# Kernel tuning notes

Hardware: AMD Instinct MI355X
Metric: run time of the kernel (lower is better)

## Reference

```python
import jax, jax.numpy as jnp
import numpy as np
from jax import lax

B, UNITS, IN_DIM = 1024, 4096, 256
CHI = 4  # forced: scatter writes 16 = chi*chi values per pair


def setup_inputs() -> dict:
    key = jax.random.key(0)
    k1, k2, k3 = jax.random.split(key, 3)
    inputs = jax.random.normal(k1, (B, IN_DIM), dtype=jnp.float32)
    W = jax.random.normal(k2, (UNITS, IN_DIM), dtype=jnp.float32) * 0.5  # sigma=0.5
    b = 2.0 * jnp.pi * jax.random.uniform(k3, (UNITS,), dtype=jnp.float32)
    return {"inputs": inputs, "W": W, "b": b}


def reference(inputs, W, b):
    # theta: [B, U]
    theta = inputs @ W.T + b
    half = theta * 0.5
    c = jnp.cos(half) ** 2          # R00 (real)
    s = jnp.sin(half) ** 2          # R11 (real)
    o = jnp.sin(theta) * 0.5        # imag part of R01
    z = jnp.zeros_like(c)
    R00 = lax.complex(c, z)
    R01 = lax.complex(z, o)
    R10 = lax.complex(z, -o)
    R11 = lax.complex(s, z)
    # R: [B, U, 2, 2] single-qubit rotation matrix per unit
    R = jnp.stack([jnp.stack([R00, R01], -1), jnp.stack([R10, R11], -1)], -2)
    A = R[:, 0::2]   # [B, K, 2, 2], K = U/2
    Bm = R[:, 1::2]  # [B, K, 2, 2]
    # kron(A, Bm)[2a+c, 2b+d] = A[a,b] * Bm[c,d] -> axes (a,c,b,d) then reshape
    kron = (A[:, :, :, None, :, None] * Bm[:, :, None, :, None, :]).reshape(
        A.shape[0], A.shape[1], CHI, CHI)
    # original returns (batch, chi, chi, units/2)
    return jnp.transpose(kron, (0, 2, 3, 1))
```

## Files before the change

### kernel.cpp

```cpp
#include <hip/hip_runtime.h>

#define IND   256
#define KC    32
#define WGRP  12
#define WROW  (16 * WGRP)

__global__ __launch_bounds__(256, 2)
void FeatureEncodingLayer_30374008718005_kernel(
        const float* __restrict__ X,
        const float* __restrict__ W,
        const float* __restrict__ bias,
        float* __restrict__ outf)
{
    __shared__ float Xs[KC][64];
    __shared__ float Ws[KC][WROW];

    const int tid = threadIdx.x;
    const int tx  = tid & 15;
    const int ty  = tid >> 4;

    const int kq  = tid & 7;
    const int rr  = tid >> 3;
    const int vsw = kq << 2;

    const int pt = blockIdx.x & 31;
    const int bt = blockIdx.x >> 5;

    const int b0 = bt * 64;
    const int p0 = pt * 64;
    const int u0 = p0 * 2;

    float acc[4][8];
#pragma unroll
    for (int i = 0; i < 4; ++i)
#pragma unroll
        for (int j = 0; j < 8; ++j) acc[i][j] = 0.f;

    for (int c = 0; c < IND / KC; ++c) {
        if (c) __syncthreads();
#pragma unroll
        for (int j = 0; j < 2; ++j) {
            const int r = rr + 32 * j;
            const float4 v = *reinterpret_cast<const float4*>(
                X + (size_t)(b0 + r) * IND + c * KC + kq * 4);
            const int col = r ^ vsw;
            Xs[kq * 4 + 0][col] = v.x;
            Xs[kq * 4 + 1][col] = v.y;
            Xs[kq * 4 + 2][col] = v.z;
            Xs[kq * 4 + 3][col] = v.w;
        }
#pragma unroll
        for (int j = 0; j < 4; ++j) {
            const int u = rr + 32 * j;
            const float4 v = *reinterpret_cast<const float4*>(
                W + (size_t)(u0 + u) * IND + c * KC + kq * 4);
            const int col = ((u >> 3) * WGRP + (u & 7)) ^ vsw;
            Ws[kq * 4 + 0][col] = v.x;
            Ws[kq * 4 + 1][col] = v.y;
            Ws[kq * 4 + 2][col] = v.z;
            Ws[kq * 4 + 3][col] = v.w;
        }
        __syncthreads();
#pragma unroll 8
        for (int k = 0; k < KC; ++k) {
            const int vr = ((k >> 2) & 7) << 2;
            const float4 xv = *reinterpret_cast<const float4*>(&Xs[k][(ty * 4) ^ vr]);
            const float4 wa = *reinterpret_cast<const float4*>(&Ws[k][(tx * WGRP) ^ vr]);
            const float4 wb = *reinterpret_cast<const float4*>(&Ws[k][(tx * WGRP + 4) ^ vr]);
            const float xr[4] = {xv.x, xv.y, xv.z, xv.w};
            const float wv[8] = {wa.x, wa.y, wa.z, wa.w, wb.x, wb.y, wb.z, wb.w};
#pragma unroll
            for (int rb = 0; rb < 4; ++rb)
#pragma unroll
                for (int i = 0; i < 8; ++i)
                    acc[rb][i] = fmaf(xr[rb], wv[i], acc[rb][i]);
        }
    }

    const float4 bva = *reinterpret_cast<const float4*>(bias + u0 + tx * 8);
    const float4 bvb = *reinterpret_cast<const float4*>(bias + u0 + tx * 8 + 4);
    const float bv[8] = {bva.x, bva.y, bva.z, bva.w, bvb.x, bvb.y, bvb.z, bvb.w};

#pragma unroll
    for (int rb = 0; rb < 4; ++rb) {
        const int b = b0 + ty * 4 + rb;
        float ca[4], sa[4], cb[4], sb[4], oo[4];
#pragma unroll
        for (int rp = 0; rp < 4; ++rp) {
            const float tA = acc[rb][2 * rp]     + bv[2 * rp];
            const float tB = acc[rb][2 * rp + 1] + bv[2 * rp + 1];
            float sA, cA, sB, cB;
            sincosf(tA, &sA, &cA);
            sincosf(tB, &sB, &cB);
            ca[rp] = 0.5f * (1.f + cA);
            sa[rp] = 0.5f * (1.f - cA);
            cb[rp] = 0.5f * (1.f + cB);
            sb[rp] = 0.5f * (1.f - cB);
            oo[rp] = 0.25f * sA * sB;
        }
        float* bp = outf + (size_t)b * 32768 + p0 + tx * 4;

#define STORE4(rc, EXPR) do {                                   \
        float4 v_;                                              \
        { const int rp = 0; v_.x = (EXPR); }                    \
        { const int rp = 1; v_.y = (EXPR); }                    \
        { const int rp = 2; v_.z = (EXPR); }                    \
        { const int rp = 3; v_.w = (EXPR); }                    \
        *reinterpret_cast<float4*>(bp + (rc) * 2048) = v_;      \
    } while (0)

        STORE4(0,  ca[rp] * cb[rp]);
        STORE4(1,  0.f);
        STORE4(2,  0.f);
        STORE4(3,  -oo[rp]);
        STORE4(4,  0.f);
        STORE4(5,  ca[rp] * sb[rp]);
        STORE4(6,  oo[rp]);
        STORE4(7,  0.f);
        STORE4(8,  0.f);
        STORE4(9,  oo[rp]);
        STORE4(10, sa[rp] * cb[rp]);
        STORE4(11, 0.f);
        STORE4(12, -oo[rp]);
        STORE4(13, 0.f);
        STORE4(14, 0.f);
        STORE4(15, sa[rp] * sb[rp]);
#undef STORE4
    }
}

extern "C" void kernel_launch(void* const* d_in, const int* in_sizes, int n_in,
                              void* d_out, int out_size, void* d_ws, size_t ws_size,
                              hipStream_t stream) {
    const float* X  = (const float*)d_in[0];
    const float* W  = (const float*)d_in[1];
    const float* bv = (const float*)d_in[2];

    FeatureEncodingLayer_30374008718005_kernel<<<dim3(512), dim3(256), 0, stream>>>(
        X, W, bv, (float*)d_out);
}
```

Measured before the change: 50.26 us.

## Shrink blocks to 64 threads with 8x8 register tiles and fast sincos

Changes the GEMM tiling from 256-thread blocks that compute 64x128 tiles with 4x8 per-thread outputs to 64-thread blocks that compute 64x64 tiles with 8x8 per-thread outputs, over 1024 blocks. Global loads are batched into registers before the shared-memory stores, and the swizzle is changed to match. sincosf is replaced by the fast __sincosf intrinsic. The larger register tile raises register pressure and leaves fewer waves per CU, which can hide latency less well. The fast intrinsic also loses accuracy for large arguments.

```diff
diff --git a/kernel.cpp b/kernel.cpp
--- a/kernel.cpp
+++ b/kernel.cpp
@@ -1,11 +1,9 @@
 #include <hip/hip_runtime.h>
 
-#define IND   256
-#define KC    32
-#define WGRP  12
-#define WROW  (16 * WGRP)
+#define IND 256
+#define KC  32
 
-__global__ __launch_bounds__(256, 2)
+__global__ __launch_bounds__(64, 2)
 void FeatureEncodingLayer_30374008718005_kernel(
         const float* __restrict__ X,
         const float* __restrict__ W,
@@ -13,67 +11,79 @@
         float* __restrict__ outf)
 {
     __shared__ float Xs[KC][64];
-    __shared__ float Ws[KC][WROW];
+    __shared__ float Ws[KC][64];
 
     const int tid = threadIdx.x;
-    const int tx  = tid & 15;
-    const int ty  = tid >> 4;
+    const int tx  = tid & 7;
+    const int ty  = tid >> 3;
 
     const int kq  = tid & 7;
     const int rr  = tid >> 3;
-    const int vsw = kq << 2;
+    const int sw  = kq << 3;
 
-    const int pt = blockIdx.x & 31;
-    const int bt = blockIdx.x >> 5;
-
+    const int pt = blockIdx.x & 63;
+    const int bt = blockIdx.x >> 6;
     const int b0 = bt * 64;
-    const int p0 = pt * 64;
+    const int p0 = pt * 32;
     const int u0 = p0 * 2;
 
-    float acc[4][8];
+    float acc[8][8];
 #pragma unroll
-    for (int i = 0; i < 4; ++i)
+    for (int i = 0; i < 8; ++i)
 #pragma unroll
         for (int j = 0; j < 8; ++j) acc[i][j] = 0.f;
 
     for (int c = 0; c < IND / KC; ++c) {
         if (c) __syncthreads();
+
+        float4 vx[8];
 #pragma unroll
-        for (int j = 0; j < 2; ++j) {
-            const int r = rr + 32 * j;
-            const float4 v = *reinterpret_cast<const float4*>(
+        for (int j = 0; j < 8; ++j) {
+            const int r = rr + 8 * j;
+            vx[j] = *reinterpret_cast<const float4*>(
                 X + (size_t)(b0 + r) * IND + c * KC + kq * 4);
-            const int col = r ^ vsw;
-            Xs[kq * 4 + 0][col] = v.x;
-            Xs[kq * 4 + 1][col] = v.y;
-            Xs[kq * 4 + 2][col] = v.z;
-            Xs[kq * 4 + 3][col] = v.w;
         }
 #pragma unroll
-        for (int j = 0; j < 4; ++j) {
-            const int u = rr + 32 * j;
-            const float4 v = *reinterpret_cast<const float4*>(
+        for (int j = 0; j < 8; ++j) {
+            const int col = (rr + 8 * j) ^ sw;
+            Xs[kq * 4 + 0][col] = vx[j].x;
+            Xs[kq * 4 + 1][col] = vx[j].y;
+            Xs[kq * 4 + 2][col] = vx[j].z;
+            Xs[kq * 4 + 3][col] = vx[j].w;
+        }
+        float4 vw[8];
+#pragma unroll
+        for (int j = 0; j < 8; ++j) {
+            const int u = rr + 8 * j;
+            vw[j] = *reinterpret_cast<const float4*>(
                 W + (size_t)(u0 + u) * IND + c * KC + kq * 4);
-            const int col = ((u >> 3) * WGRP + (u & 7)) ^ vsw;
-            Ws[kq * 4 + 0][col] = v.x;
-            Ws[kq * 4 + 1][col] = v.y;
-            Ws[kq * 4 + 2][col] = v.z;
-            Ws[kq * 4 + 3][col] = v.w;
+        }
+#pragma unroll
+        for (int j = 0; j < 8; ++j) {
+            const int col = (rr + 8 * j) ^ sw;
+            Ws[kq * 4 + 0][col] = vw[j].x;
+            Ws[kq * 4 + 1][col] = vw[j].y;
+            Ws[kq * 4 + 2][col] = vw[j].z;
+            Ws[kq * 4 + 3][col] = vw[j].w;
         }
         __syncthreads();
-#pragma unroll 8
+
+#pragma unroll 4
         for (int k = 0; k < KC; ++k) {
-            const int vr = ((k >> 2) & 7) << 2;
-            const float4 xv = *reinterpret_cast<const float4*>(&Xs[k][(ty * 4) ^ vr]);
-            const float4 wa = *reinterpret_cast<const float4*>(&Ws[k][(tx * WGRP) ^ vr]);
-            const float4 wb = *reinterpret_cast<const float4*>(&Ws[k][(tx * WGRP + 4) ^ vr]);
-            const float xr[4] = {xv.x, xv.y, xv.z, xv.w};
-            const float wv[8] = {wa.x, wa.y, wa.z, wa.w, wb.x, wb.y, wb.z, wb.w};
+            const int g  = (k >> 2) << 3;
+            const int xc = (ty * 8) ^ g;
+            const int wc = (tx * 8) ^ g;
+            const float4 x0 = *reinterpret_cast<const float4*>(&Xs[k][xc]);
+            const float4 x1 = *reinterpret_cast<const float4*>(&Xs[k][xc + 4]);
+            const float4 w0 = *reinterpret_cast<const float4*>(&Ws[k][wc]);
+            const float4 w1 = *reinterpret_cast<const float4*>(&Ws[k][wc + 4]);
+            const float xr[8] = {x0.x, x0.y, x0.z, x0.w, x1.x, x1.y, x1.z, x1.w};
+            const float wv[8] = {w0.x, w0.y, w0.z, w0.w, w1.x, w1.y, w1.z, w1.w};
 #pragma unroll
-            for (int rb = 0; rb < 4; ++rb)
+            for (int i = 0; i < 8; ++i)
 #pragma unroll
-                for (int i = 0; i < 8; ++i)
-                    acc[rb][i] = fmaf(xr[rb], wv[i], acc[rb][i]);
+                for (int j = 0; j < 8; ++j)
+                    acc[i][j] = fmaf(xr[i], wv[j], acc[i][j]);
         }
     }
 
@@ -82,16 +92,16 @@
     const float bv[8] = {bva.x, bva.y, bva.z, bva.w, bvb.x, bvb.y, bvb.z, bvb.w};
 
 #pragma unroll
-    for (int rb = 0; rb < 4; ++rb) {
-        const int b = b0 + ty * 4 + rb;
+    for (int rb = 0; rb < 8; ++rb) {
+        const int b = b0 + ty * 8 + rb;
         float ca[4], sa[4], cb[4], sb[4], oo[4];
 #pragma unroll
         for (int rp = 0; rp < 4; ++rp) {
             const float tA = acc[rb][2 * rp]     + bv[2 * rp];
             const float tB = acc[rb][2 * rp + 1] + bv[2 * rp + 1];
             float sA, cA, sB, cB;
-            sincosf(tA, &sA, &cA);
-            sincosf(tB, &sB, &cB);
+            __sincosf(tA, &sA, &cA);
+            __sincosf(tB, &sB, &cB);
             ca[rp] = 0.5f * (1.f + cA);
             sa[rp] = 0.5f * (1.f - cA);
             cb[rp] = 0.5f * (1.f + cB);
@@ -136,6 +146,6 @@
     const float* W  = (const float*)d_in[1];
     const float* bv = (const float*)d_in[2];
 
-    FeatureEncodingLayer_30374008718005_kernel<<<dim3(512), dim3(256), 0, stream>>>(
+    FeatureEncodingLayer_30374008718005_kernel<<<dim3(1024), dim3(64), 0, stream>>>(
         X, W, bv, (float*)d_out);
 }
```

New measurement: 58.79 us. 17.0% more time.
